# Kernel tuning notes

Measured on AMD Instinct MI355X. Metric: run time of the kernel, lower is better.

The kernel has to match this reference:

```python
import jax, jax.numpy as jnp
import numpy as np

B, T, IN, H, OUT = 4096, 28, 28, 1024, 10


def setup_inputs() -> dict:
    key = jax.random.key(0)
    ks = jax.random.split(key, 6)
    s_ih = 1.0 / np.sqrt(IN)
    s_h = 1.0 / np.sqrt(H)
    return {
        "x": jax.random.normal(ks[0], (B, T, IN), dtype=jnp.float32),
        "W_ih": jax.random.uniform(ks[1], (IN, 4 * H), jnp.float32, -s_ih, s_ih),
        "W_hh": jax.random.uniform(ks[2], (H, 4 * H), jnp.float32, -s_h, s_h),
        "b": jax.random.uniform(ks[3], (4 * H,), jnp.float32, -s_h, s_h),
        "Wc": jax.random.uniform(ks[4], (H, OUT), jnp.float32, -s_h, s_h),
        "bc": jax.random.uniform(ks[5], (OUT,), jnp.float32, -s_h, s_h),
    }


def _lstm_last_hidden(x, W_ih, W_hh, b):
    # Precompute input projections for all timesteps: [T, B, 4H]
    xg = jnp.einsum('bti,ig->tbg', x, W_ih) + b
    h0 = jnp.zeros((x.shape[0], W_hh.shape[0]), x.dtype)
    c0 = jnp.zeros_like(h0)

    def step(carry, xg_t):
        h, c = carry
        gates = xg_t + h @ W_hh  # [B, 4H]
        i, f, g, o = jnp.split(gates, 4, axis=-1)
        i = jax.nn.sigmoid(i)
        f = jax.nn.sigmoid(f)
        g = jnp.tanh(g)
        o = jax.nn.sigmoid(o)
        c = f * c + i * g
        h = o * jnp.tanh(c)
        return (h, c), None

    (h, _), _ = jax.lax.scan(step, (h0, c0), xg)
    return h


def reference(x, W_ih, W_hh, b, Wc, bc):
    h = _lstm_last_hidden(x, W_ih, W_hh, b)
    # dropout is identity at inference (eval mode)
    return h @ Wc + bc
```

## Files before the change

### kernel.cpp

```cpp
#include <hip/hip_runtime.h>
#include <stdint.h>

#define GLOBAL_AS __attribute__((address_space(1)))
#define LDS_AS    __attribute__((address_space(3)))

typedef __attribute__((ext_vector_type(8))) short  short8;
typedef __attribute__((ext_vector_type(4))) float  floatx4;

static constexpr int B_   = 4096;
static constexpr int T_   = 28;
static constexpr int IN_  = 28;
static constexpr int H_   = 1024;
static constexpr int G4_  = 4096;
static constexpr int OUT_ = 10;
static constexpr int NT_  = 16;

__device__ __forceinline__ float bf2f(unsigned short u) {
  union { uint32_t i; float f; } v; v.i = ((uint32_t)u) << 16; return v.f;
}
__device__ __forceinline__ unsigned short f2bf(float f) {
  union { float f; uint32_t i; } v; v.f = f;
  uint32_t x = v.i;
  uint32_t lsb = (x >> 16) & 1u;
  x += 0x7fffu + lsb;
  return (unsigned short)(x >> 16);
}
__device__ __forceinline__ float sigm(float x) {
  return __builtin_amdgcn_rcpf(1.f + __builtin_amdgcn_exp2f(-1.4426950408889634f * x));
}
__device__ __forceinline__ float tanh_f(float x) {
  return 1.f - 2.f * __builtin_amdgcn_rcpf(1.f + __builtin_amdgcn_exp2f(2.8853900817779268f * x));
}
__device__ __forceinline__ void stage16(const unsigned short* g, unsigned short* l) {
  __builtin_amdgcn_global_load_lds(
      (const GLOBAL_AS uint32_t*)g, (LDS_AS uint32_t*)l, 16, 0, 0);
}

__global__ __launch_bounds__(256) void conv_x_kernel(const float* __restrict__ x,
                                                     unsigned short* __restrict__ xb) {
  int row = blockIdx.x * 256 + threadIdx.x;
  int t  = row >> 12;
  int bb = row & 4095;
  const float* src = x + (bb * T_ + t) * IN_;
  unsigned short* dst = xb + row * 32;
#pragma unroll
  for (int k = 0; k < IN_; ++k) dst[k] = f2bf(src[k]);
  dst[28] = 0; dst[29] = 0; dst[30] = 0; dst[31] = 0;
}

__global__ __launch_bounds__(256) void perm_whh_kernel(const float* __restrict__ whh,
                                                       unsigned short* __restrict__ wp) {
  __shared__ float lds[64][17];
  int g64  = blockIdx.x >> 2;
  int gate = blockIdx.x & 3;
  int oc0  = gate * H_ + g64 * 16;
  int n0   = g64 * 64 + gate * 16;
  int tid  = threadIdx.x;
  for (int kc = 0; kc < 16; ++kc) {
    int k0 = kc * 64;
    __syncthreads();
#pragma unroll
    for (int e = 0; e < 4; ++e) {
      int idx = e * 256 + tid;
      int k = idx >> 4, cc = idx & 15;
      lds[k][cc] = whh[(k0 + k) * G4_ + oc0 + cc];
    }
    __syncthreads();
#pragma unroll
    for (int e = 0; e < 4; ++e) {
      int idx = e * 256 + tid;
      int n = idx >> 6, kk = idx & 63;
      wp[(n0 + n) * H_ + k0 + kk] = f2bf(lds[kk][n]);
    }
  }
}

__global__ __launch_bounds__(256) void perm_wih_kernel(const float* __restrict__ wih,
                                                       unsigned short* __restrict__ wip) {
  __shared__ float lds[28][17];
  int g64  = blockIdx.x >> 2;
  int gate = blockIdx.x & 3;
  int oc0  = gate * H_ + g64 * 16;
  int n0   = g64 * 64 + gate * 16;
  int tid  = threadIdx.x;
  for (int idx = tid; idx < 448; idx += 256) {
    int k = idx >> 4, cc = idx & 15;
    lds[k][cc] = wih[k * G4_ + oc0 + cc];
  }
  __syncthreads();
#pragma unroll
  for (int e = 0; e < 2; ++e) {
    int idx = e * 256 + tid;
    int n = idx >> 5, kk = idx & 31;
    wip[(n0 + n) * 32 + kk] = (kk < IN_) ? f2bf(lds[kk][n]) : (unsigned short)0;
  }
}

__global__ __launch_bounds__(512, 2) void lstm_step_kernel(
    const unsigned short* __restrict__ hprev,
    const unsigned short* __restrict__ wp,
    const unsigned short* __restrict__ xbt,
    const unsigned short* __restrict__ wip,
    const float* __restrict__ bias,
    float* __restrict__ cst,
    unsigned short* __restrict__ hnext,
    int first) {
  __shared__ __align__(16) unsigned short lds[65536];

  const int tid = threadIdx.x;
  const int w   = tid >> 6;
  const int l   = tid & 63;
  const int wm  = w >> 2;
  const int wn  = w & 3;
  const int lc  = l & 15;
  const int lk  = l >> 4;

  const int hid = blockIdx.x;
  const int lid = (hid & 7) * 32 + (hid >> 3);
  const int bx  = lid & 15, by = lid >> 4;
  const int m0  = bx * 256;
  const int n0  = by * 256;

  const int swz  = (lc & 7) << 4;
  const int swzx = (lc & 3) << 4;

  const int r8  = tid >> 3;
  const int c8  = (tid & 7) * 8;
  const int c8s = c8 ^ ((r8 & 7) * 8);
  const size_t aoff = (size_t)(m0 + r8) * H_ + c8s;
  const int bwn_low = r8 >> 5;
  const int bc31    = r8 & 31;
  const int rx   = tid >> 2;
  const int cx8  = (tid & 3) * 8;
  const int cx8s = cx8 ^ ((rx & 3) * 8);

  auto stageA = [&](int bufu, int kt, int i) {
    stage16(hprev + aoff + (size_t)i * (64 * H_) + kt * 64,
            lds + bufu + i * 4096 + tid * 8);
  };
  auto stageB = [&](int bufu, int kt, int j) {
    int col = n0 + (((j & 1) * 2 + bwn_low) * 64) + ((j >> 1) * 32) + bc31;
    stage16(wp + (size_t)col * H_ + c8s + kt * 64,
            lds + bufu + 16384 + j * 4096 + tid * 8);
  };
  auto stageXA = [&](int half) {
    int row = half * 128 + rx;
    stage16(xbt + (size_t)(m0 + row) * 32 + cx8s,
            lds + 32768 + half * 4096 + tid * 8);
  };
  auto stageXB = [&](int half) {
    int col = n0 + (rx >> 5) * 64 + half * 32 + (rx & 31);
    stage16(wip + (size_t)col * 32 + cx8s,
            lds + 32768 + 8192 + half * 4096 + tid * 8);
  };
  auto ldsr = [&](int byteoff) -> short8 {
    return *reinterpret_cast<const short8*>(reinterpret_cast<const char*>(lds) + byteoff);
  };

  floatx4 acc[8][4];
#pragma unroll
  for (int i = 0; i < 8; ++i)
#pragma unroll
    for (int j = 0; j < 4; ++j) acc[i][j] = (floatx4){0.f, 0.f, 0.f, 0.f};

  short8 a[4][2], b[2][2];

#define LOAD_A(PB, MH)                                                               \
  _Pragma("unroll") for (int m_ = 0; m_ < 4; ++m_)                                   \
  _Pragma("unroll") for (int k_ = 0; k_ < 2; ++k_)                                   \
    a[m_][k_] = ldsr((PB) + (wm * 128 + (MH) * 64 + m_ * 16 + lc) * 128 +            \
                     ((k_ * 64 + lk * 16) ^ swz));

#define LOAD_B(PB, NH)                                                               \
  _Pragma("unroll") for (int n_ = 0; n_ < 2; ++n_)                                   \
  _Pragma("unroll") for (int k_ = 0; k_ < 2; ++k_)                                   \
    b[n_][k_] = ldsr((PB) + 32768 + ((NH) * 128 + wn * 32 + n_ * 16 + lc) * 128 +    \
                     ((k_ * 64 + lk * 16) ^ swz));

#define MFMA_Q(MH, NH)                                                               \
  __builtin_amdgcn_s_barrier();                                                      \
  asm volatile("s_waitcnt lgkmcnt(0)" ::: "memory");                                 \
  __builtin_amdgcn_sched_barrier(0);                                                 \
  __builtin_amdgcn_s_setprio(1);                                                     \
  _Pragma("unroll") for (int m_ = 0; m_ < 4; ++m_)                                   \
  _Pragma("unroll") for (int n_ = 0; n_ < 2; ++n_)                                   \
  _Pragma("unroll") for (int k_ = 0; k_ < 2; ++k_)                                   \
    acc[(MH) * 4 + m_][(NH) * 2 + n_] = __builtin_amdgcn_mfma_f32_16x16x32_bf16(     \
        a[m_][k_], b[n_][k_], acc[(MH) * 4 + m_][(NH) * 2 + n_], 0, 0, 0);           \
  __builtin_amdgcn_s_setprio(0);                                                     \
  __builtin_amdgcn_sched_barrier(0);

#define TRAIL_BARRIER                                                                \
  __builtin_amdgcn_s_barrier();                                                      \
  __builtin_amdgcn_sched_barrier(0);

  if (first) {
    stageXA(0); stageXA(1); stageXB(0); stageXB(1);
    asm volatile("s_waitcnt vmcnt(0)" ::: "memory");
    __builtin_amdgcn_s_barrier();
    __builtin_amdgcn_sched_barrier(0);
    short8 xb4[4];
#pragma unroll
    for (int nf = 0; nf < 4; ++nf)
      xb4[nf] = ldsr(65536 + 16384 +
                     ((nf >> 1) * 128 + wn * 32 + (nf & 1) * 16 + lc) * 64 +
                     ((lk * 16) ^ swzx));
#pragma unroll
    for (int mf = 0; mf < 8; ++mf) {
      short8 xa = ldsr(65536 + (wm * 128 + mf * 16 + lc) * 64 + ((lk * 16) ^ swzx));
#pragma unroll
      for (int nf = 0; nf < 4; ++nf)
        acc[mf][nf] = __builtin_amdgcn_mfma_f32_16x16x32_bf16(xa, xb4[nf], acc[mf][nf], 0, 0, 0);
    }
  } else {
    stageXA(0); stageXA(1); stageXB(0); stageXB(1);
#pragma unroll
    for (int i = 0; i < 4; ++i) stageA(0, 0, i);
#pragma unroll
    for (int j = 0; j < 4; ++j) stageB(0, 0, j);
    asm volatile("s_waitcnt vmcnt(8)" ::: "memory");
    __builtin_amdgcn_s_barrier();
    __builtin_amdgcn_sched_barrier(0);
    {
      short8 xb4[4];
#pragma unroll
      for (int nf = 0; nf < 4; ++nf)
        xb4[nf] = ldsr(65536 + 16384 +
                       ((nf >> 1) * 128 + wn * 32 + (nf & 1) * 16 + lc) * 64 +
                       ((lk * 16) ^ swzx));
      __builtin_amdgcn_s_setprio(1);
#pragma unroll
      for (int mf = 0; mf < 8; ++mf) {
        short8 xa = ldsr(65536 + (wm * 128 + mf * 16 + lc) * 64 + ((lk * 16) ^ swzx));
#pragma unroll
        for (int nf = 0; nf < 4; ++nf)
          acc[mf][nf] = __builtin_amdgcn_mfma_f32_16x16x32_bf16(xa, xb4[nf], acc[mf][nf], 0, 0, 0);
      }
      __builtin_amdgcn_s_setprio(0);
      asm volatile("s_waitcnt lgkmcnt(0)" ::: "memory");
      __builtin_amdgcn_sched_barrier(0);
    }
    __builtin_amdgcn_s_barrier();
    __builtin_amdgcn_sched_barrier(0);
    stageA(32768, 1, 0); stageA(32768, 1, 2);
    stageB(32768, 1, 2); stageB(32768, 1, 3);
    stageA(32768, 1, 1); stageA(32768, 1, 3);
    asm volatile("s_waitcnt vmcnt(6)" ::: "memory");
    __builtin_amdgcn_s_barrier();
    __builtin_amdgcn_sched_barrier(0);

    for (int kt = 0; kt < NT_; ++kt) {
      const int pbB = (kt & 1) * 65536;
      const int pbu = (kt & 1) * 32768;
      const int qbu = ((kt + 1) & 1) * 32768;

      LOAD_A(pbB, 0)
      LOAD_B(pbB, 0)
      if (kt + 1 < NT_) { stageB(qbu, kt + 1, 0); stageB(qbu, kt + 1, 1); }
      MFMA_Q(0, 0)
      TRAIL_BARRIER

      LOAD_B(pbB, 1)
      if (kt + 2 < NT_) { stageA(pbu, kt + 2, 0); stageA(pbu, kt + 2, 2); }
      MFMA_Q(0, 1)
      TRAIL_BARRIER

      LOAD_A(pbB, 1)
      if (kt + 2 < NT_) { stageB(pbu, kt + 2, 2); stageB(pbu, kt + 2, 3); }
      MFMA_Q(1, 1)
      TRAIL_BARRIER

      LOAD_B(pbB, 0)
      if (kt + 2 < NT_) { stageA(pbu, kt + 2, 1); stageA(pbu, kt + 2, 3); }
      MFMA_Q(1, 0)
      if (kt == NT_ - 2) { asm volatile("s_waitcnt vmcnt(0)" ::: "memory"); }
      else               { asm volatile("s_waitcnt vmcnt(6)" ::: "memory"); }
      TRAIL_BARRIER
    }
  }

  const int jj  = (by * 4 + wn) * 16 + lc;
  const float bi  = bias[jj];
  const float bf_ = bias[H_ + jj];
  const float bg_ = bias[2 * H_ + jj];
  const float bo_ = bias[3 * H_ + jj];
#pragma unroll
  for (int mf = 0; mf < 8; ++mf) {
    const int rbase = m0 + wm * 128 + mf * 16 + lk * 4;
#pragma unroll
    for (int r = 0; r < 4; ++r) {
      const size_t idx = (size_t)(rbase + r) * H_ + jj;
      float ig = sigm(acc[mf][0][r] + bi);
      float fg = sigm(acc[mf][1][r] + bf_);
      float gg = tanh_f(acc[mf][2][r] + bg_);
      float og = sigm(acc[mf][3][r] + bo_);
      float cp = first ? 0.f : cst[idx];
      float cn = fg * cp + ig * gg;
      cst[idx] = cn;
      hnext[idx] = f2bf(og * tanh_f(cn));
    }
  }
#undef LOAD_A
#undef LOAD_B
#undef MFMA_Q
#undef TRAIL_BARRIER
}

__global__ __launch_bounds__(256) void cls_kernel(const unsigned short* __restrict__ h,
                                                  const float* __restrict__ wc,
                                                  const float* __restrict__ bc,
                                                  float* __restrict__ out) {
  int w = threadIdx.x >> 6, l = threadIdx.x & 63;
  int row = blockIdx.x * 4 + w;
  float acc[OUT_];
#pragma unroll
  for (int o = 0; o < OUT_; ++o) acc[o] = 0.f;
  const unsigned short* hr = h + row * H_;
  for (int k = l; k < H_; k += 64) {
    float hv = bf2f(hr[k]);
#pragma unroll
    for (int o = 0; o < OUT_; ++o) acc[o] += hv * wc[k * OUT_ + o];
  }
#pragma unroll
  for (int o = 0; o < OUT_; ++o) {
    float v = acc[o];
#pragma unroll
    for (int s = 32; s > 0; s >>= 1) v += __shfl_down(v, s, 64);
    if (l == 0) out[row * OUT_ + o] = v + bc[o];
  }
}

extern "C" void kernel_launch(void* const* d_in, const int* in_sizes, int n_in,
                              void* d_out, int out_size, void* d_ws, size_t ws_size,
                              hipStream_t stream) {
  const float* x    = (const float*)d_in[0];
  const float* wih  = (const float*)d_in[1];
  const float* whh  = (const float*)d_in[2];
  const float* bias = (const float*)d_in[3];
  const float* wc   = (const float*)d_in[4];
  const float* bc   = (const float*)d_in[5];
  float* out = (float*)d_out;

  char* ws = (char*)d_ws;
  unsigned short* wp  = (unsigned short*)(ws);
  unsigned short* wip = (unsigned short*)(ws + 8388608);
  unsigned short* xb  = (unsigned short*)(ws + 8650752);
  unsigned short* h0  = (unsigned short*)(ws + 15990784);
  unsigned short* h1  = (unsigned short*)(ws + 24379392);
  float*          cst = (float*)(ws + 32768000);

  hipLaunchKernelGGL(conv_x_kernel,  dim3(448), dim3(256), 0, stream, x, xb);
  hipLaunchKernelGGL(perm_whh_kernel, dim3(256), dim3(256), 0, stream, whh, wp);
  hipLaunchKernelGGL(perm_wih_kernel, dim3(256), dim3(256), 0, stream, wih, wip);

  unsigned short* hb[2] = {h0, h1};
  for (int t = 0; t < T_; ++t) {
    unsigned short* hn = hb[t & 1];
    unsigned short* hp = hb[(t & 1) ^ 1];
    hipLaunchKernelGGL(lstm_step_kernel, dim3(256), dim3(512), 0, stream,
                       hp, wp, xb + (size_t)t * (B_ * 32), wip, bias, cst, hn,
                       (t == 0) ? 1 : 0);
  }
  hipLaunchKernelGGL(cls_kernel, dim3(1024), dim3(256), 0, stream, hb[1], wc, bc, out);
}
```

Baseline: 1.144 ms.

## Software-pipeline LDS fragment loads ahead of MFMA with register double-buffering

Restructures the recurrent GEMM main loop so that LDS fragment reads for the next quadrant are issued before the current quadrant's MFMAs. It uses separate register sets (a0/a1, b0e/b0o/b1) and unrolls by two k-tiles to alternate buffers. It drops the pre-MFMA barrier and lgkmcnt wait, replacing them with a single vmcnt-gated barrier per phase, and precomputes LDS base offsets. This is meant to hide LDS latency and cut barrier count, at the cost of more VGPR pressure and a more fragile hazard ordering around buffer reuse.

```diff
diff --git a/kernel.cpp b/kernel.cpp
--- a/kernel.cpp
+++ b/kernel.cpp
@@ -157,48 +157,51 @@
     return *reinterpret_cast<const short8*>(reinterpret_cast<const char*>(lds) + byteoff);
   };
 
+  const int vaA0 = (wm * 128 + lc) * 128 + ((lk * 16) ^ swz);
+  const int vaA1 = (wm * 128 + lc) * 128 + ((64 + lk * 16) ^ swz);
+  const int vaB0 = 32768 + (wn * 32 + lc) * 128 + ((lk * 16) ^ swz);
+  const int vaB1 = 32768 + (wn * 32 + lc) * 128 + ((64 + lk * 16) ^ swz);
+
   floatx4 acc[8][4];
 #pragma unroll
   for (int i = 0; i < 8; ++i)
 #pragma unroll
     for (int j = 0; j < 4; ++j) acc[i][j] = (floatx4){0.f, 0.f, 0.f, 0.f};
 
-  short8 a[4][2], b[2][2];
-
-#define LOAD_A(PB, MH)                                                               \
-  _Pragma("unroll") for (int m_ = 0; m_ < 4; ++m_)                                   \
-  _Pragma("unroll") for (int k_ = 0; k_ < 2; ++k_)                                   \
-    a[m_][k_] = ldsr((PB) + (wm * 128 + (MH) * 64 + m_ * 16 + lc) * 128 +            \
-                     ((k_ * 64 + lk * 16) ^ swz));
-
-#define LOAD_B(PB, NH)                                                               \
-  _Pragma("unroll") for (int n_ = 0; n_ < 2; ++n_)                                   \
-  _Pragma("unroll") for (int k_ = 0; k_ < 2; ++k_)                                   \
-    b[n_][k_] = ldsr((PB) + 32768 + ((NH) * 128 + wn * 32 + n_ * 16 + lc) * 128 +    \
-                     ((k_ * 64 + lk * 16) ^ swz));
-
-#define MFMA_Q(MH, NH)                                                               \
-  __builtin_amdgcn_s_barrier();                                                      \
-  asm volatile("s_waitcnt lgkmcnt(0)" ::: "memory");                                 \
-  __builtin_amdgcn_sched_barrier(0);                                                 \
-  __builtin_amdgcn_s_setprio(1);                                                     \
-  _Pragma("unroll") for (int m_ = 0; m_ < 4; ++m_)                                   \
-  _Pragma("unroll") for (int n_ = 0; n_ < 2; ++n_)                                   \
-  _Pragma("unroll") for (int k_ = 0; k_ < 2; ++k_)                                   \
-    acc[(MH) * 4 + m_][(NH) * 2 + n_] = __builtin_amdgcn_mfma_f32_16x16x32_bf16(     \
-        a[m_][k_], b[n_][k_], acc[(MH) * 4 + m_][(NH) * 2 + n_], 0, 0, 0);           \
-  __builtin_amdgcn_s_setprio(0);                                                     \
+  short8 a0[4][2], a1[4][2], b0e[2][2], b0o[2][2], b1[2][2];
+
+#define LOAD_A_TO(ARR, PB, MH)                                                   \
+  _Pragma("unroll") for (int m_ = 0; m_ < 4; ++m_) {                             \
+    ARR[m_][0] = ldsr((PB) + vaA0 + ((MH) * 64 + m_ * 16) * 128);                \
+    ARR[m_][1] = ldsr((PB) + vaA1 + ((MH) * 64 + m_ * 16) * 128);                \
+  }
+#define LOAD_B_TO(ARR, PB, NH)                                                   \
+  _Pragma("unroll") for (int n_ = 0; n_ < 2; ++n_) {                             \
+    ARR[n_][0] = ldsr((PB) + vaB0 + ((NH) * 128 + n_ * 16) * 128);               \
+    ARR[n_][1] = ldsr((PB) + vaB1 + ((NH) * 128 + n_ * 16) * 128);               \
+  }
+#define MFMA_Q(AR, BR, MH, NH)                                                   \
+  __builtin_amdgcn_s_setprio(1);                                                 \
+  _Pragma("unroll") for (int m_ = 0; m_ < 4; ++m_)                               \
+  _Pragma("unroll") for (int n_ = 0; n_ < 2; ++n_)                               \
+  _Pragma("unroll") for (int k_ = 0; k_ < 2; ++k_)                               \
+    acc[(MH) * 4 + m_][(NH) * 2 + n_] = __builtin_amdgcn_mfma_f32_16x16x32_bf16( \
+        AR[m_][k_], BR[n_][k_], acc[(MH) * 4 + m_][(NH) * 2 + n_], 0, 0, 0);     \
+  __builtin_amdgcn_s_setprio(0);
+#define PHASE_END                                                                \
+  asm volatile("s_waitcnt vmcnt(8)" ::: "memory");                               \
+  __builtin_amdgcn_sched_barrier(0);                                             \
+  __builtin_amdgcn_s_barrier();                                                  \
   __builtin_amdgcn_sched_barrier(0);
-
-#define TRAIL_BARRIER                                                                \
-  __builtin_amdgcn_s_barrier();                                                      \
+#define HARD_SYNC(VM)                                                            \
+  asm volatile("s_waitcnt vmcnt(" #VM ")" ::: "memory");                         \
+  __builtin_amdgcn_sched_barrier(0);                                             \
+  __builtin_amdgcn_s_barrier();                                                  \
   __builtin_amdgcn_sched_barrier(0);
 
   if (first) {
     stageXA(0); stageXA(1); stageXB(0); stageXB(1);
-    asm volatile("s_waitcnt vmcnt(0)" ::: "memory");
-    __builtin_amdgcn_s_barrier();
-    __builtin_amdgcn_sched_barrier(0);
+    HARD_SYNC(0)
     short8 xb4[4];
 #pragma unroll
     for (int nf = 0; nf < 4; ++nf)
@@ -215,12 +218,10 @@
   } else {
     stageXA(0); stageXA(1); stageXB(0); stageXB(1);
 #pragma unroll
+    for (int j = 0; j < 4; ++j) stageB(0, 0, j);
+#pragma unroll
     for (int i = 0; i < 4; ++i) stageA(0, 0, i);
-#pragma unroll
-    for (int j = 0; j < 4; ++j) stageB(0, 0, j);
-    asm volatile("s_waitcnt vmcnt(8)" ::: "memory");
-    __builtin_amdgcn_s_barrier();
-    __builtin_amdgcn_sched_barrier(0);
+    HARD_SYNC(8)
     {
       short8 xb4[4];
 #pragma unroll
@@ -242,40 +243,51 @@
     }
     __builtin_amdgcn_s_barrier();
     __builtin_amdgcn_sched_barrier(0);
-    stageA(32768, 1, 0); stageA(32768, 1, 2);
-    stageB(32768, 1, 2); stageB(32768, 1, 3);
-    stageA(32768, 1, 1); stageA(32768, 1, 3);
-    asm volatile("s_waitcnt vmcnt(6)" ::: "memory");
+#pragma unroll
+    for (int j = 0; j < 4; ++j) stageB(32768, 1, j);
+#pragma unroll
+    for (int i = 0; i < 4; ++i) stageA(32768, 1, i);
+    HARD_SYNC(8)
+    LOAD_A_TO(a0, 0, 0)
+    LOAD_B_TO(b0e, 0, 0)
+    asm volatile("s_waitcnt lgkmcnt(0)" ::: "memory");
+    __builtin_amdgcn_sched_barrier(0);
     __builtin_amdgcn_s_barrier();
     __builtin_amdgcn_sched_barrier(0);
 
-    for (int kt = 0; kt < NT_; ++kt) {
-      const int pbB = (kt & 1) * 65536;
-      const int pbu = (kt & 1) * 32768;
-      const int qbu = ((kt + 1) & 1) * 32768;
-
-      LOAD_A(pbB, 0)
-      LOAD_B(pbB, 0)
-      if (kt + 1 < NT_) { stageB(qbu, kt + 1, 0); stageB(qbu, kt + 1, 1); }
-      MFMA_Q(0, 0)
-      TRAIL_BARRIER
-
-      LOAD_B(pbB, 1)
-      if (kt + 2 < NT_) { stageA(pbu, kt + 2, 0); stageA(pbu, kt + 2, 2); }
-      MFMA_Q(0, 1)
-      TRAIL_BARRIER
-
-      LOAD_A(pbB, 1)
-      if (kt + 2 < NT_) { stageB(pbu, kt + 2, 2); stageB(pbu, kt + 2, 3); }
-      MFMA_Q(1, 1)
-      TRAIL_BARRIER
-
-      LOAD_B(pbB, 0)
-      if (kt + 2 < NT_) { stageA(pbu, kt + 2, 1); stageA(pbu, kt + 2, 3); }
-      MFMA_Q(1, 0)
-      if (kt == NT_ - 2) { asm volatile("s_waitcnt vmcnt(0)" ::: "memory"); }
-      else               { asm volatile("s_waitcnt vmcnt(6)" ::: "memory"); }
-      TRAIL_BARRIER
+    for (int kt = 0; kt < NT_; kt += 2) {
+      if (kt + 2 < NT_) { stageB(0, kt + 2, 0); stageB(0, kt + 2, 1); }
+      LOAD_B_TO(b1, 0, 1)
+      MFMA_Q(a0, b0e, 0, 0)
+      PHASE_END
+      if (kt + 2 < NT_) { stageA(0, kt + 2, 0); stageA(0, kt + 2, 1); }
+      LOAD_A_TO(a1, 0, 1)
+      MFMA_Q(a0, b1, 0, 1)
+      PHASE_END
+      if (kt + 2 < NT_) { stageB(0, kt + 2, 2); stageB(0, kt + 2, 3); }
+      LOAD_B_TO(b0o, 65536, 0)
+      MFMA_Q(a1, b1, 1, 1)
+      PHASE_END
+      if (kt + 2 < NT_) { stageA(0, kt + 2, 2); stageA(0, kt + 2, 3); }
+      LOAD_A_TO(a0, 65536, 0)
+      MFMA_Q(a1, b0e, 1, 0)
+      PHASE_END
+      if (kt + 3 < NT_) { stageB(32768, kt + 3, 0); stageB(32768, kt + 3, 1); }
+      LOAD_B_TO(b1, 65536, 1)
+      MFMA_Q(a0, b0o, 0, 0)
+      PHASE_END
+      if (kt + 3 < NT_) { stageA(32768, kt + 3, 0); stageA(32768, kt + 3, 1); }
+      LOAD_A_TO(a1, 65536, 1)
+      MFMA_Q(a0, b1, 0, 1)
+      PHASE_END
+      if (kt + 3 < NT_) { stageB(32768, kt + 3, 2); stageB(32768, kt + 3, 3); }
+      LOAD_B_TO(b0e, 0, 0)
+      MFMA_Q(a1, b1, 1, 1)
+      PHASE_END
+      if (kt + 3 < NT_) { stageA(32768, kt + 3, 2); stageA(32768, kt + 3, 3); }
+      LOAD_A_TO(a0, 0, 0)
+      MFMA_Q(a1, b0o, 1, 0)
+      PHASE_END
     }
   }
 
@@ -300,10 +312,11 @@
       hnext[idx] = f2bf(og * tanh_f(cn));
     }
   }
-#undef LOAD_A
-#undef LOAD_B
+#undef LOAD_A_TO
+#undef LOAD_B_TO
 #undef MFMA_Q
-#undef TRAIL_BARRIER
+#undef PHASE_END
+#undef HARD_SYNC
 }
 
 __global__ __launch_bounds__(256) void cls_kernel(const unsigned short* __restrict__ h,
```

Result: slower. 1.689 ms (+47.7%).
